# Kernel tuning notes

Hardware: AMD Instinct MI355X
Metric: run time of the kernel (lower is better)

The kernel has to match this reference:

```python
import jax, jax.numpy as jnp
import numpy as np
import math

B, S, D, H, DFF = 4, 2048, 1024, 16, 4096
DK = D // H
EPS = 1e-5

def setup_inputs() -> dict:
    key = jax.random.key(0)
    ks = jax.random.split(key, 16)
    s_d = 1.0 / math.sqrt(D)
    s_ff = 1.0 / math.sqrt(DFF)
    return {
        "x": jax.random.normal(ks[0], (B, S, D), jnp.float32),
        "wq": jax.random.uniform(ks[1], (D, D), jnp.float32, -s_d, s_d),
        "bq": jnp.zeros((D,), jnp.float32),
        "wk": jax.random.uniform(ks[2], (D, D), jnp.float32, -s_d, s_d),
        "bk": jnp.zeros((D,), jnp.float32),
        "wv": jax.random.uniform(ks[3], (D, D), jnp.float32, -s_d, s_d),
        "bv": jnp.zeros((D,), jnp.float32),
        "wo": jax.random.uniform(ks[4], (D, D), jnp.float32, -s_d, s_d),
        "bo": jnp.zeros((D,), jnp.float32),
        "w1": jax.random.uniform(ks[5], (DFF, D), jnp.float32, -s_d, s_d),
        "b1": jnp.zeros((DFF,), jnp.float32),
        "w2": jax.random.uniform(ks[6], (D, DFF), jnp.float32, -s_ff, s_ff),
        "b2": jnp.zeros((D,), jnp.float32),
        "ln1_g": jnp.ones((D,), jnp.float32),
        "ln1_b": jnp.zeros((D,), jnp.float32),
        "ln2_g": jnp.ones((D,), jnp.float32),
        "ln2_b": jnp.zeros((D,), jnp.float32),
    }

def _layernorm(x, g, b):
    mu = jnp.mean(x, axis=-1, keepdims=True)
    var = jnp.mean(jnp.square(x - mu), axis=-1, keepdims=True)
    return (x - mu) * jax.lax.rsqrt(var + EPS) * g + b

def reference(x, wq, bq, wk, bk, wv, bv, wo, bo, w1, b1, w2, b2, ln1_g, ln1_b, ln2_g, ln2_b):
    # Multi-head self-attention (dropout in eval mode -> identity).
    Q = (x @ wq.T + bq).reshape(B, S, H, DK).transpose(0, 2, 1, 3)  # (B,H,S,DK)
    K = (x @ wk.T + bk).reshape(B, S, H, DK).transpose(0, 2, 1, 3)
    V = (x @ wv.T + bv).reshape(B, S, H, DK).transpose(0, 2, 1, 3)
    scores = jnp.einsum('bhqd,bhkd->bhqk', Q, K) / math.sqrt(DK)  # (B,H,S,S)
    attn = jax.nn.softmax(scores, axis=-1)
    ctx = jnp.einsum('bhqk,bhkd->bhqd', attn, V)
    ctx = ctx.transpose(0, 2, 1, 3).reshape(B, S, D)
    attn_out = ctx @ wo.T + bo
    # SkipConnection: x + norm(sublayer)  (post-applied LayerNorm on sublayer output)
    x = x + _layernorm(attn_out, ln1_g, ln1_b)
    # FFN
    ff = jax.nn.relu(x @ w1.T + b1) @ w2.T + b2
    return x + _layernorm(ff, ln2_g, ln2_b)
```

## Files before the change

### kernel.cpp

```cpp
#include <hip/hip_runtime.h>
#include <hip/hip_bf16.h>
#include <stdint.h>


#define DI __device__ __forceinline__

typedef __attribute__((ext_vector_type(4))) float f32x4;
typedef __attribute__((ext_vector_type(16))) float f32x16;
typedef __attribute__((ext_vector_type(8))) short bf16x8;
typedef __attribute__((ext_vector_type(4))) short s16x4;

#define B_ 4
#define S_ 2048
#define D_ 1024
#define H_ 16
#define DK_ 64
#define DFF_ 4096
#define M_ 8192

DI float bf2f(short s) {
  union { unsigned u; float f; } v;
  v.u = ((unsigned)(unsigned short)s) << 16;
  return v.f;
}
DI short f2bf(float f) {
  union { float f; unsigned u; } v;
  v.f = f;
  unsigned r = v.u + 0x7FFFu + ((v.u >> 16) & 1u);
  return (short)(r >> 16);
}
DI unsigned pkbf(float lo, float hi) {
  unsigned r;
  asm("v_cvt_pk_bf16_f32 %0, %1, %2" : "=v"(r) : "v"(lo), "v"(hi));
  return r;
}
DI void plswap(unsigned& a, unsigned& b) {
  asm volatile("v_permlane32_swap_b32 %0, %1" : "+v"(a), "+v"(b));
}

__global__ __launch_bounds__(256) void cvt_kernel(const float* __restrict__ in,
                                                  short* __restrict__ out, int n) {
  long i = ((long)blockIdx.x * blockDim.x + threadIdx.x) * 8;
  if (i >= n) return;
  f32x4 a = *(const f32x4*)(in + i);
  f32x4 b = *(const f32x4*)(in + i + 4);
  bf16x8 r;
  r[0] = f2bf(a[0]); r[1] = f2bf(a[1]); r[2] = f2bf(a[2]); r[3] = f2bf(a[3]);
  r[4] = f2bf(b[0]); r[5] = f2bf(b[1]); r[6] = f2bf(b[2]); r[7] = f2bf(b[3]);
  *(bf16x8*)(out + i) = r;
}

DI void gl_lds16(const void* g, void* l) {
  __builtin_amdgcn_global_load_lds(
      (const __attribute__((address_space(1))) unsigned int*)g,
      (__attribute__((address_space(3))) unsigned int*)l, 16, 0, 0);
}

template <int MODE>
__global__ __launch_bounds__(256, 2)
void gemm_bt(const short* __restrict__ A, const short* __restrict__ Bm,
             const float* __restrict__ bias0, const float* __restrict__ bias1,
             const float* __restrict__ bias2, short* __restrict__ C,
             int M, int N, int K,
             short* __restrict__ Qo, short* __restrict__ Ko, short* __restrict__ Vo) {
  __shared__ short As[128 * 32];
  __shared__ short Bs[128 * 32];
  const int t = threadIdx.x, w = t >> 6, l = t & 63;
  const int row0 = blockIdx.y * 128, col0 = blockIdx.x * 128;
  const int wr = (w >> 1) * 64, wc = (w & 1) * 64;
  const int lr = l & 15, lk = l >> 4;

  f32x4 acc[4][4] = {};

  const int e0 = (w * 64 + l) * 8;
  const int e1 = ((4 + w) * 64 + l) * 8;
  const int ar0 = e0 >> 5, ac0 = e0 & 31;
  const int ar1 = e1 >> 5, ac1 = e1 & 31;
  short* la0 = &As[w * 512];
  short* la1 = &As[(4 + w) * 512];
  short* lb0 = &Bs[w * 512];
  short* lb1 = &Bs[(4 + w) * 512];
  const short* Ab = A + (long)row0 * K;
  const short* Bb = Bm + (long)col0 * K;

  for (int k0 = 0; k0 < K; k0 += 32) {
    __syncthreads();
    gl_lds16(Ab + (long)ar0 * K + k0 + ac0, la0);
    gl_lds16(Ab + (long)ar1 * K + k0 + ac1, la1);
    gl_lds16(Bb + (long)ar0 * K + k0 + ac0, lb0);
    gl_lds16(Bb + (long)ar1 * K + k0 + ac1, lb1);
    __syncthreads();
    bf16x8 af[4], bfr[4];
#pragma unroll
    for (int m = 0; m < 4; ++m)
      af[m] = *(const bf16x8*)&As[(wr + m * 16 + lr) * 32 + lk * 8];
#pragma unroll
    for (int n = 0; n < 4; ++n)
      bfr[n] = *(const bf16x8*)&Bs[(wc + n * 16 + lr) * 32 + lk * 8];
#pragma unroll
    for (int m = 0; m < 4; ++m)
#pragma unroll
      for (int n = 0; n < 4; ++n)
        acc[m][n] =
            __builtin_amdgcn_mfma_f32_16x16x32_bf16(af[m], bfr[n], acc[m][n], 0, 0, 0);
  }

  if (MODE == 2) {
    const int which = col0 >> 10;
#pragma unroll
    for (int m = 0; m < 4; ++m) {
#pragma unroll
      for (int n = 0; n < 4; ++n) {
        const int r0 = row0 + wr + m * 16 + lk * 4;
        const int c = col0 + wc + n * 16 + lr;
        const int cc = c & 1023;
        const int h = cc >> 6, dk = cc & 63;
        const int bb = r0 >> 11, s = r0 & 2047;
        if (which == 2) {
          const float bias = bias2[cc];
          s16x4 v4;
#pragma unroll
          for (int j = 0; j < 4; ++j) v4[j] = f2bf(acc[m][n][j] + bias);
          *(s16x4*)(Vo + ((long)((bb * H_ + h) * DK_ + dk)) * S_ + s) = v4;
        } else {
          const float bias = (which == 0 ? bias0[cc] : bias1[cc]);
          const float sc = (which == 0 ? 0.125f : 1.0f);
          short* dst = (which == 0 ? Qo : Ko);
#pragma unroll
          for (int j = 0; j < 4; ++j)
            dst[(((long)(bb * H_ + h) * S_) + s + j) * DK_ + dk] =
                f2bf((acc[m][n][j] + bias) * sc);
        }
      }
    }
  } else {
#pragma unroll
    for (int m = 0; m < 4; ++m) {
#pragma unroll
      for (int n = 0; n < 4; ++n) {
#pragma unroll
        for (int j = 0; j < 4; ++j) {
          int r = row0 + wr + m * 16 + lk * 4 + j;
          int c = col0 + wc + n * 16 + lr;
          float v = acc[m][n][j] + bias0[c];
          if (MODE == 1) v = fmaxf(v, 0.0f);
          C[(long)r * N + c] = f2bf(v);
        }
      }
    }
  }
}

__global__ __launch_bounds__(256, 3)
void attn_kernel(const short* __restrict__ Q, const short* __restrict__ K,
                 const short* __restrict__ Vt, short* __restrict__ ctx) {
  __shared__ short Ks[64 * 64];
  __shared__ short Vs[64 * 64];
  const int t = threadIdx.x, w = t >> 6, l = t & 63;
  const int q31 = l & 31, hi = l >> 5;
  const int bh = blockIdx.y;
  const int q0 = blockIdx.x * 128 + w * 32;
  const long base = (long)bh * S_ * DK_;

  bf16x8 qf[4];
  {
    const short* qp = Q + base + (long)(q0 + q31) * DK_ + hi * 8;
#pragma unroll
    for (int ks = 0; ks < 4; ++ks) qf[ks] = *(const bf16x8*)(qp + ks * 16);
  }

  f32x16 oa[2] = {};
  float mrun = -1e30f, lrun = 0.0f;

  const int srow = l >> 3;
  const int scol = ((l & 7) ^ srow) * 8;
  short* ldsK0 = &Ks[w * 1024];
  short* ldsK1 = &Ks[w * 1024 + 512];
  short* ldsV0 = &Vs[w * 1024];
  short* ldsV1 = &Vs[w * 1024 + 512];
  const int kr0 = w * 16 + srow, kr1 = w * 16 + 8 + srow;

  for (int kv0 = 0; kv0 < S_; kv0 += 64) {
    __syncthreads();
    gl_lds16(K + base + (long)(kv0 + kr0) * DK_ + scol, ldsK0);
    gl_lds16(K + base + (long)(kv0 + kr1) * DK_ + scol, ldsK1);
    gl_lds16(Vt + base + (long)kr0 * S_ + kv0 + scol, ldsV0);
    gl_lds16(Vt + base + (long)kr1 * S_ + kv0 + scol, ldsV1);
    __syncthreads();

    f32x16 sacc[2] = {};
#pragma unroll
    for (int m = 0; m < 2; ++m) {
      const int row = m * 32 + q31;
      const int sw = row & 7;
#pragma unroll
      for (int ks = 0; ks < 4; ++ks) {
        bf16x8 kf = *(const bf16x8*)&Ks[row * 64 + (((2 * ks + hi) ^ sw) << 3)];
        sacc[m] = __builtin_amdgcn_mfma_f32_32x32x16_bf16(kf, qf[ks], sacc[m], 0, 0, 0);
      }
    }

    float tm = sacc[0][0];
#pragma unroll
    for (int r = 1; r < 16; ++r) tm = fmaxf(tm, sacc[0][r]);
#pragma unroll
    for (int r = 0; r < 16; ++r) tm = fmaxf(tm, sacc[1][r]);
    tm = fmaxf(tm, __shfl_xor(tm, 32, 64));
    const float mnew = fmaxf(mrun, tm);
    const float fac = __expf(mrun - mnew);
    float ps = 0.0f;
#pragma unroll
    for (int m = 0; m < 2; ++m)
#pragma unroll
      for (int r = 0; r < 16; ++r) {
        float p = __expf(sacc[m][r] - mnew);
        sacc[m][r] = p;
        ps += p;
      }
    ps += __shfl_xor(ps, 32, 64);
    lrun = lrun * fac + ps;
    mrun = mnew;
#pragma unroll
    for (int m = 0; m < 2; ++m)
#pragma unroll
      for (int r = 0; r < 16; ++r) oa[m][r] *= fac;

    bf16x8 pf[4];
#pragma unroll
    for (int m = 0; m < 2; ++m)
#pragma unroll
      for (int sb = 0; sb < 2; ++sb) {
        unsigned p0 = pkbf(sacc[m][8 * sb + 0], sacc[m][8 * sb + 1]);
        unsigned p1 = pkbf(sacc[m][8 * sb + 2], sacc[m][8 * sb + 3]);
        unsigned p2 = pkbf(sacc[m][8 * sb + 4], sacc[m][8 * sb + 5]);
        unsigned p3 = pkbf(sacc[m][8 * sb + 6], sacc[m][8 * sb + 7]);
        plswap(p0, p2);
        plswap(p1, p3);
        union { unsigned u[4]; bf16x8 v; } fb;
        fb.u[0] = p0; fb.u[1] = p1; fb.u[2] = p2; fb.u[3] = p3;
        pf[2 * m + sb] = fb.v;
      }

#pragma unroll
    for (int mt = 0; mt < 2; ++mt) {
      const int row = mt * 32 + q31;
      const int sw = row & 7;
#pragma unroll
      for (int s = 0; s < 4; ++s) {
        bf16x8 vf = *(const bf16x8*)&Vs[row * 64 + (((2 * s + hi) ^ sw) << 3)];
        oa[mt] = __builtin_amdgcn_mfma_f32_32x32x16_bf16(vf, pf[s], oa[mt], 0, 0, 0);
      }
    }
  }

  const int bb2 = bh >> 4, h = bh & 15;
  const float rl = 1.0f / lrun;
  short* crow = ctx + ((long)(bb2 * S_ + q0 + q31)) * D_ + h * 64 + 4 * hi;
#pragma unroll
  for (int mt = 0; mt < 2; ++mt)
#pragma unroll
    for (int g = 0; g < 4; ++g) {
      s16x4 v4;
#pragma unroll
      for (int i = 0; i < 4; ++i) v4[i] = f2bf(oa[mt][4 * g + i] * rl);
      *(s16x4*)(crow + mt * 32 + g * 8) = v4;
    }
}

template <int RES_BF16, int OUT_BF16>
__global__ __launch_bounds__(256)
void add_ln(const void* __restrict__ resv, const short* __restrict__ a,
            const float* __restrict__ gam, const float* __restrict__ bet,
            void* __restrict__ outv) {
  const int row = blockIdx.x, t = threadIdx.x;
  const int w = t >> 6, l = t & 63;
  const long roff = (long)row * D_;
  const int c = t * 4;
  s16x4 av = *(const s16x4*)(a + roff + c);
  float v0 = bf2f(av[0]), v1 = bf2f(av[1]), v2 = bf2f(av[2]), v3 = bf2f(av[3]);
  float s = v0 + v1 + v2 + v3;
#pragma unroll
  for (int mask = 1; mask < 64; mask <<= 1) s += __shfl_xor(s, mask, 64);
  __shared__ float r1[4], r2[4];
  if (l == 0) r1[w] = s;
  __syncthreads();
  float mu = (r1[0] + r1[1] + r1[2] + r1[3]) * (1.0f / D_);
  float d0 = v0 - mu, d1 = v1 - mu, d2 = v2 - mu, d3 = v3 - mu;
  float sq = d0 * d0 + d1 * d1 + d2 * d2 + d3 * d3;
#pragma unroll
  for (int mask = 1; mask < 64; mask <<= 1) sq += __shfl_xor(sq, mask, 64);
  if (l == 0) r2[w] = sq;
  __syncthreads();
  float var = (r2[0] + r2[1] + r2[2] + r2[3]) * (1.0f / D_);
  float rs = rsqrtf(var + 1e-5f);
  float res0, res1, res2, res3;
  if (RES_BF16) {
    s16x4 rv = *(const s16x4*)((const short*)resv + roff + c);
    res0 = bf2f(rv[0]); res1 = bf2f(rv[1]); res2 = bf2f(rv[2]); res3 = bf2f(rv[3]);
  } else {
    f32x4 rv = *(const f32x4*)((const float*)resv + roff + c);
    res0 = rv[0]; res1 = rv[1]; res2 = rv[2]; res3 = rv[3];
  }
  float o0 = res0 + d0 * rs * gam[c + 0] + bet[c + 0];
  float o1 = res1 + d1 * rs * gam[c + 1] + bet[c + 1];
  float o2 = res2 + d2 * rs * gam[c + 2] + bet[c + 2];
  float o3 = res3 + d3 * rs * gam[c + 3] + bet[c + 3];
  if (OUT_BF16) {
    s16x4 ov;
    ov[0] = f2bf(o0); ov[1] = f2bf(o1); ov[2] = f2bf(o2); ov[3] = f2bf(o3);
    *(s16x4*)((short*)outv + roff + c) = ov;
  } else {
    f32x4 ov;
    ov[0] = o0; ov[1] = o1; ov[2] = o2; ov[3] = o3;
    *(f32x4*)((float*)outv + roff + c) = ov;
  }
}

extern "C" void kernel_launch(void* const* d_in, const int* in_sizes, int n_in,
                              void* d_out, int out_size, void* d_ws, size_t ws_size,
                              hipStream_t stream) {
  (void)in_sizes; (void)n_in; (void)out_size; (void)ws_size;
  const float* x   = (const float*)d_in[0];
  const float* wq  = (const float*)d_in[1];
  const float* bq  = (const float*)d_in[2];
  const float* wk  = (const float*)d_in[3];
  const float* bk  = (const float*)d_in[4];
  const float* wv  = (const float*)d_in[5];
  const float* bv  = (const float*)d_in[6];
  const float* wo  = (const float*)d_in[7];
  const float* bo  = (const float*)d_in[8];
  const float* w1  = (const float*)d_in[9];
  const float* b1  = (const float*)d_in[10];
  const float* w2  = (const float*)d_in[11];
  const float* b2  = (const float*)d_in[12];
  const float* g1  = (const float*)d_in[13];
  const float* be1 = (const float*)d_in[14];
  const float* g2  = (const float*)d_in[15];
  const float* be2 = (const float*)d_in[16];

  char* ws = (char*)d_ws;
  const long MB = 1 << 20;
  short* xb    = (short*)(ws + 0 * MB);
  short* wqkvb = (short*)(ws + 16 * MB);
  short* wob   = (short*)(ws + 22 * MB);
  short* w1b   = (short*)(ws + 24 * MB);
  short* w2b   = (short*)(ws + 32 * MB);
  short* Qb    = (short*)(ws + 40 * MB);
  short* Kb    = (short*)(ws + 56 * MB);
  short* Vtb   = (short*)(ws + 72 * MB);
  short* ctxb  = (short*)(ws + 88 * MB);
  short* aout  = (short*)(ws + 40 * MB);
  short* x1b   = (short*)(ws + 56 * MB);
  short* hid   = (short*)(ws + 88 * MB);
  short* ffb   = (short*)(ws + 72 * MB);

  auto cvt = [&](const float* in, short* out, long n) {
    cvt_kernel<<<dim3((unsigned)((n / 8 + 255) / 256)), dim3(256), 0, stream>>>(in, out, (int)n);
  };
  cvt(x, xb, (long)M_ * D_);
  cvt(wq, wqkvb + 0L * D_ * D_, (long)D_ * D_);
  cvt(wk, wqkvb + 1L * D_ * D_, (long)D_ * D_);
  cvt(wv, wqkvb + 2L * D_ * D_, (long)D_ * D_);
  cvt(wo, wob, (long)D_ * D_);
  cvt(w1, w1b, (long)DFF_ * D_);
  cvt(w2, w2b, (long)D_ * DFF_);

  gemm_bt<2><<<dim3(3072 / 128, M_ / 128), 256, 0, stream>>>(
      xb, wqkvb, bq, bk, bv, nullptr, M_, 3072, D_, Qb, Kb, Vtb);

  attn_kernel<<<dim3(S_ / 128, B_ * H_), 256, 0, stream>>>(Qb, Kb, Vtb, ctxb);

  gemm_bt<0><<<dim3(D_ / 128, M_ / 128), 256, 0, stream>>>(
      ctxb, wob, bo, nullptr, nullptr, aout, M_, D_, D_, nullptr, nullptr, nullptr);

  add_ln<0, 1><<<dim3(M_), 256, 0, stream>>>(x, aout, g1, be1, x1b);

  gemm_bt<1><<<dim3(DFF_ / 128, M_ / 128), 256, 0, stream>>>(
      x1b, w1b, b1, nullptr, nullptr, hid, M_, DFF_, D_, nullptr, nullptr, nullptr);
  gemm_bt<0><<<dim3(D_ / 128, M_ / 128), 256, 0, stream>>>(
      hid, w2b, b2, nullptr, nullptr, ffb, M_, D_, DFF_, nullptr, nullptr, nullptr);

  add_ln<1, 0><<<dim3(M_), 256, 0, stream>>>(x1b, ffb, g2, be2, d_out);
}
```

Before: 432.3 us.

## Rewrite GEMMs with 256-row tiles and 4-stage pipelining; double-buffer attention with lazy rescale

Measured after the change: 419.5 us. -3.0%, faster.

```diff
diff --git a/kernel.cpp b/kernel.cpp
--- a/kernel.cpp
+++ b/kernel.cpp
@@ -36,6 +36,11 @@
 }
 DI void plswap(unsigned& a, unsigned& b) {
   asm volatile("v_permlane32_swap_b32 %0, %1" : "+v"(a), "+v"(b));
+}
+DI float ex2(float x) {
+  float r;
+  asm("v_exp_f32 %0, %1" : "=v"(r) : "v"(x));
+  return r;
 }
 
 __global__ __launch_bounds__(256) void cvt_kernel(const float* __restrict__ in,
@@ -56,66 +61,131 @@
       (__attribute__((address_space(3))) unsigned int*)l, 16, 0, 0);
 }
 
-template <int MODE>
-__global__ __launch_bounds__(256, 2)
-void gemm_bt(const short* __restrict__ A, const short* __restrict__ Bm,
+template <int BN, int MODE>
+__global__ __launch_bounds__(512, 2)
+void gemm_qs(const short* __restrict__ A, const short* __restrict__ Bm,
              const float* __restrict__ bias0, const float* __restrict__ bias1,
              const float* __restrict__ bias2, short* __restrict__ C,
              int M, int N, int K,
              short* __restrict__ Qo, short* __restrict__ Ko, short* __restrict__ Vo) {
-  __shared__ short As[128 * 32];
-  __shared__ short Bs[128 * 32];
+  constexpr int NF = BN / 64;
+  constexpr int WN = BN / 4;
+  constexpr int ASLOT = 256 * 32;
+  constexpr int BSLOT = BN * 32;
+
+  __shared__ short As[4 * ASLOT];
+  __shared__ short Bs[4 * BSLOT];
+
   const int t = threadIdx.x, w = t >> 6, l = t & 63;
-  const int row0 = blockIdx.y * 128, col0 = blockIdx.x * 128;
-  const int wr = (w >> 1) * 64, wc = (w & 1) * 64;
+  const int wm = w >> 2, wn = w & 3;
   const int lr = l & 15, lk = l >> 4;
 
-  f32x4 acc[4][4] = {};
-
-  const int e0 = (w * 64 + l) * 8;
-  const int e1 = ((4 + w) * 64 + l) * 8;
-  const int ar0 = e0 >> 5, ac0 = e0 & 31;
-  const int ar1 = e1 >> 5, ac1 = e1 & 31;
-  short* la0 = &As[w * 512];
-  short* la1 = &As[(4 + w) * 512];
-  short* lb0 = &Bs[w * 512];
-  short* lb1 = &Bs[(4 + w) * 512];
-  const short* Ab = A + (long)row0 * K;
-  const short* Bb = Bm + (long)col0 * K;
-
-  for (int k0 = 0; k0 < K; k0 += 32) {
-    __syncthreads();
-    gl_lds16(Ab + (long)ar0 * K + k0 + ac0, la0);
-    gl_lds16(Ab + (long)ar1 * K + k0 + ac1, la1);
-    gl_lds16(Bb + (long)ar0 * K + k0 + ac0, lb0);
-    gl_lds16(Bb + (long)ar1 * K + k0 + ac1, lb1);
-    __syncthreads();
-    bf16x8 af[4], bfr[4];
+  const int gx = gridDim.x;
+  const int nwg = gx * gridDim.y;
+  const int orig = blockIdx.y * gx + blockIdx.x;
+  const int lin = (orig & 7) * (nwg >> 3) + (orig >> 3);
+  const int row0 = (lin / gx) * 256;
+  const int col0 = (lin % gx) * BN;
+
+  const int NT = K >> 5;
+
+  const int r0 = t >> 2, s0 = (((t & 3) ^ ((r0 >> 1) & 3)) << 3);
+  const int r1 = r0 + 128, s1 = (((t & 3) ^ ((r1 >> 1) & 3)) << 3);
+  const short* Asrc0 = A + (long)(row0 + r0) * K + s0;
+  const short* Asrc1 = A + (long)(row0 + r1) * K + s1;
+  const short* Bsrc0 = Bm + (long)(col0 + r0) * K + s0;
+  const short* Bsrc1 = Bm + (long)(col0 + r1) * K + s1;
+  const int d0 = t * 8, d1 = (t + 512) * 8;
+
+  auto stageA = [&](int kt) {
+    const int ko = kt << 5;
+    short* Ab = As + (kt & 3) * ASLOT;
+    gl_lds16(Asrc0 + ko, Ab + d0);
+    gl_lds16(Asrc1 + ko, Ab + d1);
+  };
+  auto stageB = [&](int kt) {
+    const int ko = kt << 5;
+    short* Bb = Bs + (kt & 3) * BSLOT;
+    gl_lds16(Bsrc0 + ko, Bb + d0);
+    if constexpr (BN == 256) gl_lds16(Bsrc1 + ko, Bb + d1);
+  };
+
+  f32x4 acc[8][NF] = {};
+
+  stageA(0); stageB(0);
+  stageA(1); stageB(1);
+  stageA(2); stageB(2);
+
+  for (int kt = 0; kt < NT; ++kt) {
+    if (kt + 2 < NT) {
+      if constexpr (BN == 256) asm volatile("s_waitcnt vmcnt(8)" ::: "memory");
+      else                     asm volatile("s_waitcnt vmcnt(6)" ::: "memory");
+    } else if (kt + 1 < NT) {
+      if constexpr (BN == 256) asm volatile("s_waitcnt vmcnt(4)" ::: "memory");
+      else                     asm volatile("s_waitcnt vmcnt(3)" ::: "memory");
+    } else {
+      asm volatile("s_waitcnt vmcnt(0)" ::: "memory");
+    }
+    __builtin_amdgcn_s_barrier();
+
+    const short* aw = As + (kt & 3) * ASLOT + wm * (128 * 32);
+    const short* bw = Bs + (kt & 3) * BSLOT + wn * (WN * 32);
+
+    bf16x8 afr[4], bfr[NF];
+#pragma unroll
+    for (int m = 0; m < 4; ++m) {
+      const int rr = m * 16 + lr;
+      afr[m] = *(const bf16x8*)(aw + rr * 32 + ((lk ^ ((rr >> 1) & 3)) << 3));
+    }
+#pragma unroll
+    for (int n = 0; n < NF; ++n) {
+      const int rr = n * 16 + lr;
+      bfr[n] = *(const bf16x8*)(bw + rr * 32 + ((lk ^ ((rr >> 1) & 3)) << 3));
+    }
+    if (kt + 3 < NT) stageA(kt + 3);
+    __builtin_amdgcn_s_barrier();
+    asm volatile("s_waitcnt lgkmcnt(0)" ::: "memory");
+    __builtin_amdgcn_sched_barrier(0);
+    __builtin_amdgcn_s_setprio(1);
 #pragma unroll
     for (int m = 0; m < 4; ++m)
-      af[m] = *(const bf16x8*)&As[(wr + m * 16 + lr) * 32 + lk * 8];
-#pragma unroll
-    for (int n = 0; n < 4; ++n)
-      bfr[n] = *(const bf16x8*)&Bs[(wc + n * 16 + lr) * 32 + lk * 8];
+#pragma unroll
+      for (int n = 0; n < NF; ++n)
+        acc[m][n] =
+            __builtin_amdgcn_mfma_f32_16x16x32_bf16(afr[m], bfr[n], acc[m][n], 0, 0, 0);
+    __builtin_amdgcn_s_setprio(0);
+
+    bf16x8 af2[4];
+#pragma unroll
+    for (int m = 0; m < 4; ++m) {
+      const int rr = 64 + m * 16 + lr;
+      af2[m] = *(const bf16x8*)(aw + rr * 32 + ((lk ^ ((rr >> 1) & 3)) << 3));
+    }
+    if (kt + 3 < NT) stageB(kt + 3);
+    __builtin_amdgcn_s_barrier();
+    asm volatile("s_waitcnt lgkmcnt(0)" ::: "memory");
+    __builtin_amdgcn_sched_barrier(0);
+    __builtin_amdgcn_s_setprio(1);
 #pragma unroll
     for (int m = 0; m < 4; ++m)
 #pragma unroll
-      for (int n = 0; n < 4; ++n)
-        acc[m][n] =
-            __builtin_amdgcn_mfma_f32_16x16x32_bf16(af[m], bfr[n], acc[m][n], 0, 0, 0);
+      for (int n = 0; n < NF; ++n)
+        acc[4 + m][n] =
+            __builtin_amdgcn_mfma_f32_16x16x32_bf16(af2[m], bfr[n], acc[4 + m][n], 0, 0, 0);
+    __builtin_amdgcn_s_setprio(0);
   }
 
   if (MODE == 2) {
     const int which = col0 >> 10;
 #pragma unroll
-    for (int m = 0; m < 4; ++m) {
-#pragma unroll
-      for (int n = 0; n < 4; ++n) {
-        const int r0 = row0 + wr + m * 16 + lk * 4;
-        const int c = col0 + wc + n * 16 + lr;
+    for (int m = 0; m < 8; ++m) {
+#pragma unroll
+      for (int n = 0; n < NF; ++n) {
+        const int r0e = row0 + wm * 128 + m * 16 + lk * 4;
+        const int c = col0 + wn * WN + n * 16 + lr;
         const int cc = c & 1023;
         const int h = cc >> 6, dk = cc & 63;
-        const int bb = r0 >> 11, s = r0 & 2047;
+        const int bb = r0e >> 11, s = r0e & 2047;
         if (which == 2) {
           const float bias = bias2[cc];
           s16x4 v4;
@@ -124,7 +194,7 @@
           *(s16x4*)(Vo + ((long)((bb * H_ + h) * DK_ + dk)) * S_ + s) = v4;
         } else {
           const float bias = (which == 0 ? bias0[cc] : bias1[cc]);
-          const float sc = (which == 0 ? 0.125f : 1.0f);
+          const float sc = (which == 0 ? 0.1803368801f : 1.0f);
           short* dst = (which == 0 ? Qo : Ko);
 #pragma unroll
           for (int j = 0; j < 4; ++j)
@@ -135,13 +205,13 @@
     }
   } else {
 #pragma unroll
-    for (int m = 0; m < 4; ++m) {
-#pragma unroll
-      for (int n = 0; n < 4; ++n) {
+    for (int m = 0; m < 8; ++m) {
+#pragma unroll
+      for (int n = 0; n < NF; ++n) {
 #pragma unroll
         for (int j = 0; j < 4; ++j) {
-          int r = row0 + wr + m * 16 + lk * 4 + j;
-          int c = col0 + wc + n * 16 + lr;
+          const int r = row0 + wm * 128 + m * 16 + lk * 4 + j;
+          const int c = col0 + wn * WN + n * 16 + lr;
           float v = acc[m][n][j] + bias0[c];
           if (MODE == 1) v = fmaxf(v, 0.0f);
           C[(long)r * N + c] = f2bf(v);
@@ -151,11 +221,11 @@
   }
 }
 
-__global__ __launch_bounds__(256, 3)
+__global__ __launch_bounds__(256, 4)
 void attn_kernel(const short* __restrict__ Q, const short* __restrict__ K,
                  const short* __restrict__ Vt, short* __restrict__ ctx) {
-  __shared__ short Ks[64 * 64];
-  __shared__ short Vs[64 * 64];
+  __shared__ short Ks[2 * 64 * 64];
+  __shared__ short Vs[2 * 64 * 64];
   const int t = threadIdx.x, w = t >> 6, l = t & 63;
   const int q31 = l & 31, hi = l >> 5;
   const int bh = blockIdx.y;
@@ -174,19 +244,26 @@
 
   const int srow = l >> 3;
   const int scol = ((l & 7) ^ srow) * 8;
-  short* ldsK0 = &Ks[w * 1024];
-  short* ldsK1 = &Ks[w * 1024 + 512];
-  short* ldsV0 = &Vs[w * 1024];
-  short* ldsV1 = &Vs[w * 1024 + 512];
   const int kr0 = w * 16 + srow, kr1 = w * 16 + 8 + srow;
-
-  for (int kv0 = 0; kv0 < S_; kv0 += 64) {
-    __syncthreads();
-    gl_lds16(K + base + (long)(kv0 + kr0) * DK_ + scol, ldsK0);
-    gl_lds16(K + base + (long)(kv0 + kr1) * DK_ + scol, ldsK1);
-    gl_lds16(Vt + base + (long)kr0 * S_ + kv0 + scol, ldsV0);
-    gl_lds16(Vt + base + (long)kr1 * S_ + kv0 + scol, ldsV1);
-    __syncthreads();
+  const int lw0 = w * 1024, lw1 = w * 1024 + 512;
+
+  gl_lds16(K + base + (long)kr0 * DK_ + scol, &Ks[lw0]);
+  gl_lds16(K + base + (long)kr1 * DK_ + scol, &Ks[lw1]);
+  gl_lds16(Vt + base + (long)kr0 * S_ + scol, &Vs[lw0]);
+  gl_lds16(Vt + base + (long)kr1 * S_ + scol, &Vs[lw1]);
+
+  for (int tt = 0; tt < 32; ++tt) {
+    asm volatile("s_waitcnt vmcnt(0)" ::: "memory");
+    __builtin_amdgcn_s_barrier();
+    if (tt + 1 < 32) {
+      const int kb = ((tt + 1) & 1) * 4096;
+      const int kvn = (tt + 1) * 64;
+      gl_lds16(K + base + (long)(kvn + kr0) * DK_ + scol, &Ks[kb + lw0]);
+      gl_lds16(K + base + (long)(kvn + kr1) * DK_ + scol, &Ks[kb + lw1]);
+      gl_lds16(Vt + base + (long)kr0 * S_ + kvn + scol, &Vs[kb + lw0]);
+      gl_lds16(Vt + base + (long)kr1 * S_ + kvn + scol, &Vs[kb + lw1]);
+    }
+    const int cb = (tt & 1) * 4096;
 
     f32x16 sacc[2] = {};
 #pragma unroll
@@ -195,35 +272,45 @@
       const int sw = row & 7;
 #pragma unroll
       for (int ks = 0; ks < 4; ++ks) {
-        bf16x8 kf = *(const bf16x8*)&Ks[row * 64 + (((2 * ks + hi) ^ sw) << 3)];
+        bf16x8 kf = *(const bf16x8*)&Ks[cb + row * 64 + (((2 * ks + hi) ^ sw) << 3)];
         sacc[m] = __builtin_amdgcn_mfma_f32_32x32x16_bf16(kf, qf[ks], sacc[m], 0, 0, 0);
       }
     }
 
-    float tm = sacc[0][0];
-#pragma unroll
-    for (int r = 1; r < 16; ++r) tm = fmaxf(tm, sacc[0][r]);
-#pragma unroll
-    for (int r = 0; r < 16; ++r) tm = fmaxf(tm, sacc[1][r]);
+    float mx[8];
+#pragma unroll
+    for (int r = 0; r < 8; ++r)
+      mx[r] = fmaxf(fmaxf(sacc[0][r], sacc[0][r + 8]),
+                    fmaxf(sacc[1][r], sacc[1][r + 8]));
+    mx[0] = fmaxf(mx[0], mx[4]); mx[1] = fmaxf(mx[1], mx[5]);
+    mx[2] = fmaxf(mx[2], mx[6]); mx[3] = fmaxf(mx[3], mx[7]);
+    float tm = fmaxf(fmaxf(mx[0], mx[1]), fmaxf(mx[2], mx[3]));
     tm = fmaxf(tm, __shfl_xor(tm, 32, 64));
-    const float mnew = fmaxf(mrun, tm);
-    const float fac = __expf(mrun - mnew);
-    float ps = 0.0f;
+
+    if (!__all(tm <= mrun + 8.0f)) {
+      const float mnew = fmaxf(mrun, tm);
+      const float fac = ex2(mrun - mnew);
+      lrun *= fac;
+#pragma unroll
+      for (int m = 0; m < 2; ++m)
+#pragma unroll
+        for (int r = 0; r < 16; ++r) oa[m][r] *= fac;
+      mrun = mnew;
+    }
+
 #pragma unroll
     for (int m = 0; m < 2; ++m)
 #pragma unroll
-      for (int r = 0; r < 16; ++r) {
-        float p = __expf(sacc[m][r] - mnew);
-        sacc[m][r] = p;
-        ps += p;
-      }
+      for (int r = 0; r < 16; ++r) sacc[m][r] = ex2(sacc[m][r] - mrun);
+
+    float sm[8];
+#pragma unroll
+    for (int r = 0; r < 8; ++r)
+      sm[r] = (sacc[0][r] + sacc[0][r + 8]) + (sacc[1][r] + sacc[1][r + 8]);
+    sm[0] += sm[4]; sm[1] += sm[5]; sm[2] += sm[6]; sm[3] += sm[7];
+    float ps = (sm[0] + sm[1]) + (sm[2] + sm[3]);
     ps += __shfl_xor(ps, 32, 64);
-    lrun = lrun * fac + ps;
-    mrun = mnew;
-#pragma unroll
-    for (int m = 0; m < 2; ++m)
-#pragma unroll
-      for (int r = 0; r < 16; ++r) oa[m][r] *= fac;
+    lrun += ps;
 
     bf16x8 pf[4];
 #pragma unroll
@@ -247,7 +334,7 @@
       const int sw = row & 7;
 #pragma unroll
       for (int s = 0; s < 4; ++s) {
-        bf16x8 vf = *(const bf16x8*)&Vs[row * 64 + (((2 * s + hi) ^ sw) << 3)];
+        bf16x8 vf = *(const bf16x8*)&Vs[cb + row * 64 + (((2 * s + hi) ^ sw) << 3)];
         oa[mt] = __builtin_amdgcn_mfma_f32_32x32x16_bf16(vf, pf[s], oa[mt], 0, 0, 0);
       }
     }
@@ -365,19 +452,19 @@
   cvt(w1, w1b, (long)DFF_ * D_);
   cvt(w2, w2b, (long)D_ * DFF_);
 
-  gemm_bt<2><<<dim3(3072 / 128, M_ / 128), 256, 0, stream>>>(
+  gemm_qs<256, 2><<<dim3(3072 / 256, M_ / 256), 512, 0, stream>>>(
       xb, wqkvb, bq, bk, bv, nullptr, M_, 3072, D_, Qb, Kb, Vtb);
 
   attn_kernel<<<dim3(S_ / 128, B_ * H_), 256, 0, stream>>>(Qb, Kb, Vtb, ctxb);
 
-  gemm_bt<0><<<dim3(D_ / 128, M_ / 128), 256, 0, stream>>>(
+  gemm_qs<128, 0><<<dim3(D_ / 128, M_ / 256), 512, 0, stream>>>(
       ctxb, wob, bo, nullptr, nullptr, aout, M_, D_, D_, nullptr, nullptr, nullptr);
 
   add_ln<0, 1><<<dim3(M_), 256, 0, stream>>>(x, aout, g1, be1, x1b);
 
-  gemm_bt<1><<<dim3(DFF_ / 128, M_ / 128), 256, 0, stream>>>(
+  gemm_qs<256, 1><<<dim3(DFF_ / 256, M_ / 256), 512, 0, stream>>>(
       x1b, w1b, b1, nullptr, nullptr, hid, M_, DFF_, D_, nullptr, nullptr, nullptr);
-  gemm_bt<0><<<dim3(D_ / 128, M_ / 128), 256, 0, stream>>>(
+  gemm_qs<128, 0><<<dim3(D_ / 128, M_ / 256), 512, 0, stream>>>(
       hid, w2b, b2, nullptr, nullptr, ffb, M_, D_, DFF_, nullptr, nullptr, nullptr);
 
   add_ln<1, 0><<<dim3(M_), 256, 0, stream>>>(x1b, ffb, g2, be2, d_out);
```
